# Kernel optimization log

Hardware: AMD Instinct MI355X
Metric: run time of the kernel (lower is better)

## Reference

```python
import jax, jax.numpy as jnp
import numpy as np

N = 50000
NEG_SLOPE = 0.2

def _gat_layer(x, src, dst, W, a_src, a_dst, b):
    # x: [N, Fin], W: [Fin, Fout], a_src/a_dst: [Fout], b: [Fout]
    h = x @ W                                  # [N, Fout]
    alpha_src = h @ a_src                      # [N]
    alpha_dst = h @ a_dst                      # [N]
    e = alpha_src[src] + alpha_dst[dst]        # [E]
    e = jnp.where(e > 0, e, NEG_SLOPE * e)     # leaky_relu
    # segment softmax over incoming edges of each dst node
    m = jax.ops.segment_max(e, dst, num_segments=N)
    w = jnp.exp(e - m[dst])
    denom = jax.ops.segment_sum(w, dst, num_segments=N) + jnp.asarray(1e-16, e.dtype)
    alpha = w / denom[dst]                     # [E]
    out = jax.ops.segment_sum(alpha[:, None] * h[src], dst, num_segments=N)
    return out + b

def setup_inputs() -> dict:
    key = jax.random.key(0)
    ks = jax.random.split(key, 10)
    x = jax.random.normal(ks[0], (N, 128), dtype=jnp.float32)
    edge_index = jax.random.randint(ks[1], (2, 800000), 0, N, dtype=jnp.int64)
    def glorot(k, shape):
        fan = shape[0] + (shape[1] if len(shape) > 1 else 1)
        s = jnp.sqrt(6.0 / fan)
        return jax.random.uniform(k, shape, jnp.float32, -s, s)
    return {
        "x": x,
        "edge_index": edge_index,
        "W1": glorot(ks[2], (128, 64)),
        "a1_src": glorot(ks[3], (64,)),
        "a1_dst": glorot(ks[4], (64,)),
        "b1": jnp.zeros((64,), jnp.float32),
        "W2": glorot(ks[5], (64, 64)),
        "a2_src": glorot(ks[6], (64,)),
        "a2_dst": glorot(ks[7], (64,)),
        "b2": jnp.zeros((64,), jnp.float32),
    }

def reference(x, edge_index, W1, a1_src, a1_dst, b1, W2, a2_src, a2_dst, b2):
    loops = jnp.arange(N, dtype=edge_index.dtype)
    src = jnp.concatenate([edge_index[0], loops])  # add self-loops (PyG default)
    dst = jnp.concatenate([edge_index[1], loops])
    h = _gat_layer(x, src, dst, W1, a1_src, a1_dst, b1)
    h = jax.nn.relu(h)
    out = _gat_layer(h, src, dst, W2, a2_src, a2_dst, b2)
    return out
```

## Files before the change

kernel.cpp:

```cpp
#include <hip/hip_runtime.h>
#include <hip/hip_bf16.h>
#include <hip/hip_fp16.h>
#include <cstddef>


#define NNODES 50000
#define NEDGES 800000
#define FOUT   64
#define NBKT   512
#define BSPAN  98
#define CHUNK  4096
#define REGS   2560
#define NLBMAX 256

__device__ __forceinline__ float leaky(float t) { return t > 0.f ? t : 0.2f * t; }
#define RL(v, j) __builtin_amdgcn_readlane((v), (j))

using half8  = __attribute__((ext_vector_type(8))) _Float16;
using half4v = __attribute__((ext_vector_type(4))) _Float16;
using f32x4  = __attribute__((ext_vector_type(4))) float;


__global__ __launch_bounds__(256) void k_localsort(
    const int* __restrict__ ei, unsigned* __restrict__ gout,
    int* __restrict__ goff, int E)
{
    __shared__ unsigned lrec[CHUNK];
    __shared__ unsigned lsrt[CHUNK];
    __shared__ int cnt[NBKT];
    __shared__ int cur[NBKT];
    __shared__ int exc[NBKT + 1];

    const int t = threadIdx.x;
    const int blk = blockIdx.x;
    const int e0 = blk * CHUNK;
    const int e1 = min(e0 + CHUNK, E);
    const int ne = e1 - e0;

    for (int i = t; i < NBKT; i += 256) cnt[i] = 0;
    __syncthreads();

    for (int i = e0 + t; i < e1; i += 256) {
        unsigned s = (unsigned)ei[i];
        unsigned d = (unsigned)ei[E + i];
        lrec[i - e0] = s | (d << 16);
        atomicAdd(&cnt[d / BSPAN], 1);
    }
    __syncthreads();

    if (t < 64) {
        int c[8]; int s = 0;
        #pragma unroll
        for (int k = 0; k < 8; ++k) { c[k] = cnt[t * 8 + k]; s += c[k]; }
        int inc = s;
        #pragma unroll
        for (int d = 1; d < 64; d <<= 1) { int u = __shfl_up(inc, d); if (t >= d) inc += u; }
        int ex = inc - s;
        #pragma unroll
        for (int k = 0; k < 8; ++k) { exc[t * 8 + k] = ex; cur[t * 8 + k] = ex; ex += c[k]; }
        if (t == 63) exc[NBKT] = ex;
    }
    __syncthreads();

    for (int i = t; i < ne; i += 256) {
        unsigned r = lrec[i];
        unsigned d = r >> 16;
        unsigned b = d / BSPAN;
        int p = atomicAdd(&cur[b], 1);
        lsrt[p] = (r & 0xFFFFu) | ((d - b * BSPAN) << 16);
    }
    __syncthreads();

    for (int i = t; i < ne; i += 256) gout[e0 + i] = lsrt[i];
    for (int i = t; i < NBKT + 1; i += 256)
        goff[blk * (NBKT + 1) + i] = e0 + exc[i];
}


__device__ __forceinline__ void csr_body(
    char* smem, int bkt,
    const unsigned* __restrict__ gout, const int* __restrict__ goff,
    int* __restrict__ csrc, int2* __restrict__ rowse,
    int n, int nlb)
{
    unsigned* ltmp  = (unsigned*)smem;
    int* lout  = (int*)(smem + REGS * 4);
    int* lcnt  = (int*)(smem + 2 * REGS * 4);
    int* lbase = lcnt + BSPAN;
    int* lcur  = lbase + BSPAN + 1;
    int* rg0   = lcur + BSPAN;
    int* rlen  = rg0 + NLBMAX;
    int* rbase = rlen + NLBMAX;

    const int t = threadIdx.x;
    const int node0 = bkt * BSPAN;
    if (node0 >= n) return;
    const int nn = min(BSPAN, n - node0);

    for (int i = t; i < BSPAN; i += 256) lcnt[i] = (i < nn) ? 1 : 0;
    if (t < nlb) {
        int g0 = goff[t * (NBKT + 1) + bkt];
        int g1 = goff[t * (NBKT + 1) + bkt + 1];
        rg0[t] = g0;
        rlen[t] = g1 - g0;
    }
    __syncthreads();

    if (t < 64) {
        int c[4]; int s = 0;
        #pragma unroll
        for (int k = 0; k < 4; ++k) {
            int idx = t * 4 + k;
            c[k] = (idx < nlb) ? rlen[idx] : 0;
            s += c[k];
        }
        int inc = s;
        #pragma unroll
        for (int d = 1; d < 64; d <<= 1) { int u = __shfl_up(inc, d); if (t >= d) inc += u; }
        int ex = inc - s;
        #pragma unroll
        for (int k = 0; k < 4; ++k) { rbase[t * 4 + k] = ex; ex += c[k]; }
        if (t == 63) rbase[NLBMAX] = ex;
    }
    __syncthreads();

    const int tot = min(rbase[nlb], REGS - BSPAN);

    for (int i = t; i < tot; i += 256) {
        int lo = 0, hi = nlb;
        while (hi - lo > 1) {
            int mid = (lo + hi) >> 1;
            if (rbase[mid] <= i) lo = mid; else hi = mid;
        }
        ltmp[i] = gout[rg0[lo] + (i - rbase[lo])];
    }
    __syncthreads();

    for (int i = t; i < tot; i += 256) atomicAdd(&lcnt[ltmp[i] >> 16], 1);
    __syncthreads();

    if (t < 64) {
        int b0 = t * 2, b1 = t * 2 + 1;
        int c0 = (b0 < BSPAN) ? lcnt[b0] : 0;
        int c1 = (b1 < BSPAN) ? lcnt[b1] : 0;
        int s = c0 + c1;
        int inc = s;
        #pragma unroll
        for (int d = 1; d < 64; d <<= 1) { int u = __shfl_up(inc, d); if (t >= d) inc += u; }
        int ex = inc - s;
        if (b0 < BSPAN) { lbase[b0] = ex;      lcur[b0] = ex + 1; }
        if (b1 < BSPAN) { lbase[b1] = ex + c0; lcur[b1] = ex + c0 + 1; }
        if (t == 63) lbase[BSPAN] = inc;
    }
    __syncthreads();

    for (int i = t; i < nn; i += 256) lout[lbase[i]] = node0 + i;
    for (int i = t; i < tot; i += 256) {
        unsigned r = ltmp[i];
        int p = atomicAdd(&lcur[r >> 16], 1);
        lout[p] = (int)(r & 0xFFFFu);
    }
    __syncthreads();

    const int gbase = bkt * REGS;
    const int total = tot + nn;
    for (int i = t; i < total; i += 256) csrc[gbase + i] = lout[i];
    for (int i = t; i < nn; i += 256)
        rowse[node0 + i] = make_int2(gbase + lbase[i], gbase + lbase[i + 1]);
}


template <int K, typename XT>
__device__ __forceinline__ void gemm_body(
    char* smem, int bx,
    const XT* __restrict__ x, const float* __restrict__ W,
    const float* __restrict__ a_src, const float* __restrict__ a_dst,
    __half* __restrict__ h16, float* __restrict__ as_, float* __restrict__ ad_, int n)
{
    constexpr int KP = K + 8;
    _Float16* Ah = (_Float16*)smem;
    _Float16* Wf = (_Float16*)(smem + 64 * KP * 2);

    const int t    = threadIdx.x;
    const int lane = t & 63;
    const int wv   = t >> 6;
    const int n16  = lane & 15;
    const int quad = lane >> 4;
    const int r0   = bx * 64;

    for (int i = t; i < K * 64; i += 256) {
        int k = i >> 6, c = i & 63;
        Wf[((k >> 3) * 64 + c) * 8 + (k & 7)] = (_Float16)W[i];
    }
    if constexpr (sizeof(XT) == 4) {
        constexpr int KQ = K / 4;
        for (int i = t; i < 64 * KQ; i += 256) {
            int r = i / KQ, kq = i % KQ;
            int row = r0 + r;
            float4 v = make_float4(0.f, 0.f, 0.f, 0.f);
            if (row < n) v = ((const float4*)(x + (size_t)row * K))[kq];
            half4v hv = { (_Float16)v.x, (_Float16)v.y, (_Float16)v.z, (_Float16)v.w };
            *(half4v*)&Ah[r * KP + kq * 4] = hv;
        }
    } else {
        constexpr int KO = K / 8;
        for (int i = t; i < 64 * KO; i += 256) {
            int r = i / KO, ko = i % KO;
            int row = r0 + r;
            half8 hv = {};
            if (row < n) hv = *(const half8*)((const _Float16*)x + (size_t)row * K + ko * 8);
            *(half8*)&Ah[r * KP + ko * 8] = hv;
        }
    }
    __syncthreads();

    half8 bfr[K / 32][4];
    #pragma unroll
    for (int kk = 0; kk < K / 32; ++kk)
        #pragma unroll
        for (int ct = 0; ct < 4; ++ct)
            bfr[kk][ct] = *(const half8*)&Wf[((kk * 4 + quad) * 64 + ct * 16 + n16) * 8];

    f32x4 acc[4];
    #pragma unroll
    for (int ct = 0; ct < 4; ++ct) acc[ct] = (f32x4){0.f, 0.f, 0.f, 0.f};

    #pragma unroll
    for (int kk = 0; kk < K / 32; ++kk) {
        half8 a = *(const half8*)&Ah[(wv * 16 + n16) * KP + kk * 32 + quad * 8];
        #pragma unroll
        for (int ct = 0; ct < 4; ++ct)
            acc[ct] = __builtin_amdgcn_mfma_f32_16x16x32_f16(a, bfr[kk][ct], acc[ct], 0, 0, 0);
    }

    const int rowb = r0 + wv * 16 + quad * 4;
    float asv[4], adv[4];
    #pragma unroll
    for (int ct = 0; ct < 4; ++ct) {
        asv[ct] = a_src[ct * 16 + n16];
        adv[ct] = a_dst[ct * 16 + n16];
    }
    float pa[4] = {0.f, 0.f, 0.f, 0.f}, pd[4] = {0.f, 0.f, 0.f, 0.f};
    #pragma unroll
    for (int ct = 0; ct < 4; ++ct)
        #pragma unroll
        for (int r = 0; r < 4; ++r) {
            pa[r] = fmaf(acc[ct][r], asv[ct], pa[r]);
            pd[r] = fmaf(acc[ct][r], adv[ct], pd[r]);
        }
    #pragma unroll
    for (int r = 0; r < 4; ++r) {
        #pragma unroll
        for (int d = 1; d <= 8; d <<= 1) {
            pa[r] += __shfl_xor(pa[r], d);
            pd[r] += __shfl_xor(pd[r], d);
        }
    }
    if (n16 == 0) {
        #pragma unroll
        for (int r = 0; r < 4; ++r) {
            if (rowb + r < n) { as_[rowb + r] = pa[r]; ad_[rowb + r] = pd[r]; }
        }
    }

    _Float16* hh = (_Float16*)h16;
    #pragma unroll
    for (int r = 0; r < 4; ++r) {
        if (rowb + r < n) {
            #pragma unroll
            for (int ct = 0; ct < 4; ++ct)
                hh[(size_t)(rowb + r) * 64 + ct * 16 + n16] = (_Float16)acc[ct][r];
        }
    }
}


__global__ __launch_bounds__(256) void k_csr_gemm1(
    const unsigned* __restrict__ gout, const int* __restrict__ goff,
    int* __restrict__ csrc, int2* __restrict__ rowse, int nlb,
    const float* __restrict__ x, const float* __restrict__ W1,
    const float* __restrict__ a1s, const float* __restrict__ a1d,
    __half* __restrict__ h16, float* __restrict__ as_, float* __restrict__ ad_, int n)
{
    extern __shared__ __align__(16) char smem[];
    if (blockIdx.x < NBKT)
        csr_body(smem, blockIdx.x, gout, goff, csrc, rowse, n, nlb);
    else
        gemm_body<128, float>(smem, blockIdx.x - NBKT, x, W1, a1s, a1d, h16, as_, ad_, n);
}

__global__ __launch_bounds__(256) void k_gemm2(
    const __half* __restrict__ xh, const float* __restrict__ W2,
    const float* __restrict__ a2s, const float* __restrict__ a2d,
    __half* __restrict__ h16, float* __restrict__ as_, float* __restrict__ ad_, int n)
{
    extern __shared__ __align__(16) char smem[];
    gemm_body<64, _Float16>(smem, blockIdx.x, (const _Float16*)xh, W2, a2s, a2d, h16, as_, ad_, n);
}


template <bool RELU, typename OT>
__device__ __forceinline__ void agg_one(
    int node, int lane, int2* __restrict__ swrow,
    const int2* __restrict__ rowse,
    const int* __restrict__ csrc, const __half* __restrict__ h16,
    const float* __restrict__ as_, const float* __restrict__ ad_,
    const float* __restrict__ bias, OT* __restrict__ out)
{
    const int2 se = rowse[node];
    const int start = se.x;
    const int end   = se.y;
    const int deg   = end - start;
    const float adn = ad_[node];

    if (deg <= 64) {
        int s = 0;
        if (lane < deg) s = csrc[start + lane];
        swrow[lane].x = s << 6;

        const int g  = lane >> 3;
        const int fl = (lane & 7) << 3;
        const __half* __restrict__ hf = h16 + fl;
        const int niter = (deg + 7) >> 3;

        int sofs[8];
        uint4 v[8];
        #pragma unroll
        for (int j = 0; j < 8; ++j) {
            if (j < niter) {
                sofs[j] = swrow[(j << 3) + g].x;
                v[j] = *(const uint4*)(hf + sofs[j]);
            }
        }

        float e = -1e30f;
        if (lane < deg) e = leaky(as_[s] + adn);
        float w = __expf(e);
        float dsum = w;
        #pragma unroll
        for (int d = 32; d >= 1; d >>= 1) dsum += __shfl_xor(dsum, d);
        swrow[lane].y = __float_as_int(w);

        float af[8] = {0.f, 0.f, 0.f, 0.f, 0.f, 0.f, 0.f, 0.f};
        #pragma unroll
        for (int j = 0; j < 8; ++j) {
            if (j < niter) {
                float wj = __int_as_float(swrow[(j << 3) + g].y);
                unsigned uu[4] = {v[j].x, v[j].y, v[j].z, v[j].w};
                #pragma unroll
                for (int q = 0; q < 4; ++q) {
                    __half2 h2 = *(__half2*)&uu[q];
                    float2 f2 = __half22float2(h2);
                    af[2 * q]     = fmaf(wj, f2.x, af[2 * q]);
                    af[2 * q + 1] = fmaf(wj, f2.y, af[2 * q + 1]);
                }
            }
        }
        #pragma unroll
        for (int q = 0; q < 8; ++q) {
            af[q] += __shfl_xor(af[q], 8);
            af[q] += __shfl_xor(af[q], 16);
            af[q] += __shfl_xor(af[q], 32);
        }
        if (g == 0) {
            float inv = 1.f / dsum;
            float4 b0 = *(const float4*)(bias + fl);
            float4 b1 = *(const float4*)(bias + fl + 4);
            float o[8] = { fmaf(af[0], inv, b0.x), fmaf(af[1], inv, b0.y),
                           fmaf(af[2], inv, b0.z), fmaf(af[3], inv, b0.w),
                           fmaf(af[4], inv, b1.x), fmaf(af[5], inv, b1.y),
                           fmaf(af[6], inv, b1.z), fmaf(af[7], inv, b1.w) };
            if (RELU) {
                #pragma unroll
                for (int q = 0; q < 8; ++q) o[q] = fmaxf(o[q], 0.f);
            }
            if constexpr (sizeof(OT) == 2) {
                __half* op = (__half*)out + (size_t)node * 64 + fl;
                __half2 p0 = __floats2half2_rn(o[0], o[1]);
                __half2 p1 = __floats2half2_rn(o[2], o[3]);
                __half2 p2 = __floats2half2_rn(o[4], o[5]);
                __half2 p3 = __floats2half2_rn(o[6], o[7]);
                uint4 pk = { *(unsigned*)&p0, *(unsigned*)&p1, *(unsigned*)&p2, *(unsigned*)&p3 };
                *(uint4*)op = pk;
            } else {
                float* op = (float*)out + (size_t)node * 64 + fl;
                *(float4*)op       = make_float4(o[0], o[1], o[2], o[3]);
                *(float4*)(op + 4) = make_float4(o[4], o[5], o[6], o[7]);
            }
        }
    } else {
        const __half* __restrict__ hp = h16 + lane;
        float m = -1e30f;
        for (int base = start; base < end; base += 64) {
            int idx = base + lane;
            if (idx < end) m = fmaxf(m, leaky(as_[csrc[idx]] + adn));
        }
        #pragma unroll
        for (int d = 32; d >= 1; d >>= 1) m = fmaxf(m, __shfl_xor(m, d));

        float acc0 = 0.f, acc1 = 0.f, acc2 = 0.f, acc3 = 0.f, dsum = 0.f;
        for (int base = start; base < end; base += 64) {
            int idx = base + lane;
            int s = 0; float w = 0.f;
            if (idx < end) {
                s = csrc[idx];
                w = __expf(leaky(as_[s] + adn) - m);
            }
            dsum += w;
            int off = s << 6;
            int wu = __float_as_uint(w);
            int cnt = min(64, end - base);
            int cr = (cnt + 3) & ~3;
            for (int j = 0; j < cr; j += 4) {
                int   o0 = RL(off, j + 0), o1 = RL(off, j + 1);
                int   o2 = RL(off, j + 2), o3 = RL(off, j + 3);
                float w0 = __uint_as_float(RL(wu, j + 0));
                float w1 = __uint_as_float(RL(wu, j + 1));
                float w2 = __uint_as_float(RL(wu, j + 2));
                float w3 = __uint_as_float(RL(wu, j + 3));
                float v0 = __half2float(hp[o0]), v1 = __half2float(hp[o1]);
                float v2 = __half2float(hp[o2]), v3 = __half2float(hp[o3]);
                acc0 = fmaf(w0, v0, acc0);
                acc1 = fmaf(w1, v1, acc1);
                acc2 = fmaf(w2, v2, acc2);
                acc3 = fmaf(w3, v3, acc3);
            }
        }
        #pragma unroll
        for (int d = 32; d >= 1; d >>= 1) dsum += __shfl_xor(dsum, d);
        float acc = (acc0 + acc1) + (acc2 + acc3);
        float o = acc / dsum + bias[lane];
        if (RELU) o = fmaxf(o, 0.f);
        if constexpr (sizeof(OT) == 2)
            ((__half*)out)[(size_t)node * 64 + lane] = __float2half(o);
        else
            ((float*)out)[(size_t)node * 64 + lane] = o;
    }
}

template <bool RELU, typename OT>
__global__ __launch_bounds__(256) void k_aggregate(
    const int2* __restrict__ rowse,
    const int* __restrict__ csrc,
    const __half* __restrict__ h16, const float* __restrict__ as_,
    const float* __restrict__ ad_, const float* __restrict__ bias,
    OT* __restrict__ out, int n)
{
    __shared__ int2 swL[4][64];

    const int lane = threadIdx.x & 63;
    const int wid  = threadIdx.x >> 6;
    const int nodeA = (blockIdx.x * 4 + wid) * 2;
    if (nodeA >= n) return;

    const int half = lane >> 5;
    const int hl   = lane & 31;
    const int node = nodeA + half;

    const int2 se = rowse[node];
    const float adn = ad_[node];
    const int start = se.x;
    const int deg   = se.y - se.x;
    const int mdeg  = max(deg, __shfl_xor(deg, 32));

    if (mdeg <= 32) {
        int s = 0;
        const bool act = hl < deg;
        if (act) s = csrc[start + hl];
        swL[wid][lane].x = s << 6;

        const int g  = (lane >> 3) & 3;
        const int fl = (lane & 7) << 3;
        const __half* __restrict__ hf = h16 + fl;
        int nit = (deg + 3) >> 2;
        nit = max(nit, __shfl_xor(nit, 32));

        const int sbase = (half << 5) + g;
        uint4 v[8];
        #pragma unroll
        for (int j = 0; j < 8; ++j) {
            if (j < nit)
                v[j] = *(const uint4*)(hf + swL[wid][sbase + (j << 2)].x);
        }

        float e = -1e30f;
        if (act) e = leaky(as_[s] + adn);
        float w = __expf(e);
        float dsum = w;
        #pragma unroll
        for (int d = 16; d >= 1; d >>= 1) dsum += __shfl_xor(dsum, d);
        swL[wid][lane].y = __float_as_int(w);

        float af[8] = {0.f, 0.f, 0.f, 0.f, 0.f, 0.f, 0.f, 0.f};
        #pragma unroll
        for (int j = 0; j < 8; ++j) {
            if (j < nit) {
                float wj = __int_as_float(swL[wid][sbase + (j << 2)].y);
                unsigned uu[4] = {v[j].x, v[j].y, v[j].z, v[j].w};
                #pragma unroll
                for (int q = 0; q < 4; ++q) {
                    __half2 h2 = *(__half2*)&uu[q];
                    float2 f2 = __half22float2(h2);
                    af[2 * q]     = fmaf(wj, f2.x, af[2 * q]);
                    af[2 * q + 1] = fmaf(wj, f2.y, af[2 * q + 1]);
                }
            }
        }
        #pragma unroll
        for (int q = 0; q < 8; ++q) {
            af[q] += __shfl_xor(af[q], 8);
            af[q] += __shfl_xor(af[q], 16);
        }
        if (g == 0) {
            float inv = 1.f / dsum;
            float4 b0 = *(const float4*)(bias + fl);
            float4 b1 = *(const float4*)(bias + fl + 4);
            float o[8] = { fmaf(af[0], inv, b0.x), fmaf(af[1], inv, b0.y),
                           fmaf(af[2], inv, b0.z), fmaf(af[3], inv, b0.w),
                           fmaf(af[4], inv, b1.x), fmaf(af[5], inv, b1.y),
                           fmaf(af[6], inv, b1.z), fmaf(af[7], inv, b1.w) };
            if (RELU) {
                #pragma unroll
                for (int q = 0; q < 8; ++q) o[q] = fmaxf(o[q], 0.f);
            }
            if constexpr (sizeof(OT) == 2) {
                __half* op = (__half*)out + (size_t)node * 64 + fl;
                __half2 p0 = __floats2half2_rn(o[0], o[1]);
                __half2 p1 = __floats2half2_rn(o[2], o[3]);
                __half2 p2 = __floats2half2_rn(o[4], o[5]);
                __half2 p3 = __floats2half2_rn(o[6], o[7]);
                uint4 pk = { *(unsigned*)&p0, *(unsigned*)&p1, *(unsigned*)&p2, *(unsigned*)&p3 };
                *(uint4*)op = pk;
            } else {
                float* op = (float*)out + (size_t)node * 64 + fl;
                *(float4*)op       = make_float4(o[0], o[1], o[2], o[3]);
                *(float4*)(op + 4) = make_float4(o[4], o[5], o[6], o[7]);
            }
        }
    } else {
        agg_one<RELU, OT>(nodeA,     lane, swL[wid], rowse, csrc, h16, as_, ad_, bias, out);
        agg_one<RELU, OT>(nodeA + 1, lane, swL[wid], rowse, csrc, h16, as_, ad_, bias, out);
    }
}


extern "C" void kernel_launch(void* const* d_in, const int* in_sizes, int n_in,
                              void* d_out, int out_size, void* d_ws, size_t ws_size,
                              hipStream_t stream) {
    const float* x   = (const float*)d_in[0];
    const int*   ei  = (const int*)  d_in[1];
    const float* W1  = (const float*)d_in[2];
    const float* a1s = (const float*)d_in[3];
    const float* a1d = (const float*)d_in[4];
    const float* b1  = (const float*)d_in[5];
    const float* W2  = (const float*)d_in[6];
    const float* a2s = (const float*)d_in[7];
    const float* a2d = (const float*)d_in[8];
    const float* b2  = (const float*)d_in[9];
    float* out = (float*)d_out;

    const int N_ = NNODES, E_ = NEDGES;
    const int NLB = (E_ + CHUNK - 1) / CHUNK;

    char* ws = (char*)d_ws;
    size_t off = 0;
    auto alloc = [&](size_t bytes) -> void* {
        void* p = ws + off;
        off += (bytes + 255) & ~(size_t)255;
        return p;
    };
    int*      csrc     = (int*)alloc((size_t)NBKT * REGS * 4);
    int2*     rowse    = (int2*)alloc((size_t)N_ * 8);
    float*    as_      = (float*)alloc((size_t)N_ * 4);
    float*    ad_      = (float*)alloc((size_t)N_ * 4);
    __half*   h16      = (__half*)alloc((size_t)N_ * FOUT * 2);
    __half*   xr2h     = (__half*)alloc((size_t)N_ * FOUT * 2);
    unsigned* gout     = (unsigned*)alloc((size_t)E_ * 4);
    int*      goff     = (int*)alloc((size_t)NLB * (NBKT + 1) * 4);

    constexpr unsigned SM_G1 = 64 * (128 + 8) * 2 + 128 * 64 * 2;
    constexpr unsigned SM_G2 = 64 * (64 + 8) * 2  + 64 * 64 * 2;

    const int GB = (N_ + 63) / 64;
    const int AB = (N_ / 2 + 3) / 4;

    k_localsort<<<NLB, 256, 0, stream>>>(ei, gout, goff, E_);
    k_csr_gemm1<<<NBKT + GB, 256, SM_G1, stream>>>(gout, goff, csrc, rowse, NLB,
                                                   x, W1, a1s, a1d, h16, as_, ad_, N_);
    k_aggregate<true,  __half><<<AB, 256, 0, stream>>>(rowse, csrc, h16, as_, ad_, b1, xr2h, N_);
    k_gemm2<<<GB, 256, SM_G2, stream>>>(xr2h, W2, a2s, a2d, h16, as_, ad_, N_);
    k_aggregate<false, float ><<<AB, 256, 0, stream>>>(rowse, csrc, h16, as_, ad_, b2, out, N_);
}
```

Before: 154.3 us.

## Fuse layer-1 aggregation with layer-2 GEMM via LDS tile and MFMA

Replaces the separate layer-1 aggregate and gemm2 kernels with one kernel. Each block aggregates 64 nodes into an fp16 LDS tile, then multiplies that tile by W2 with MFMA and computes the layer-2 attention scalars in the same pass. This removes the global round trip of the intermediate features and one launch. It also packs two low-degree nodes per wave, with half-wave processing when both have degree at most 32, to improve lane utilisation. In exchange, each block is fixed to 64 nodes, which may reduce occupancy or load balance compared with the previous aggregate grid.

```diff
diff --git a/kernel.cpp b/kernel.cpp
--- a/kernel.cpp
+++ b/kernel.cpp
@@ -289,29 +289,15 @@
         gemm_body<128, float>(smem, blockIdx.x - NBKT, x, W1, a1s, a1d, h16, as_, ad_, n);
 }
 
-__global__ __launch_bounds__(256) void k_gemm2(
-    const __half* __restrict__ xh, const float* __restrict__ W2,
-    const float* __restrict__ a2s, const float* __restrict__ a2d,
-    __half* __restrict__ h16, float* __restrict__ as_, float* __restrict__ ad_, int n)
+
+__device__ __forceinline__ void agg_one_lds(
+    int rloc, int start, int end, float adn, int lane, int2* __restrict__ swrow,
+    const int* __restrict__ csrc, const __half* __restrict__ h16,
+    const float* __restrict__ as_, const float* __restrict__ bias,
+    _Float16* __restrict__ Ah)
 {
-    extern __shared__ __align__(16) char smem[];
-    gemm_body<64, _Float16>(smem, blockIdx.x, (const _Float16*)xh, W2, a2s, a2d, h16, as_, ad_, n);
-}
-
-
-template <bool RELU, typename OT>
-__device__ __forceinline__ void agg_one(
-    int node, int lane, int2* __restrict__ swrow,
-    const int2* __restrict__ rowse,
-    const int* __restrict__ csrc, const __half* __restrict__ h16,
-    const float* __restrict__ as_, const float* __restrict__ ad_,
-    const float* __restrict__ bias, OT* __restrict__ out)
-{
-    const int2 se = rowse[node];
-    const int start = se.x;
-    const int end   = se.y;
-    const int deg   = end - start;
-    const float adn = ad_[node];
+    constexpr int KP = 72;
+    const int deg = end - start;
 
     if (deg <= 64) {
         int s = 0;
@@ -323,15 +309,10 @@
         const __half* __restrict__ hf = h16 + fl;
         const int niter = (deg + 7) >> 3;
 
-        int sofs[8];
         uint4 v[8];
         #pragma unroll
-        for (int j = 0; j < 8; ++j) {
-            if (j < niter) {
-                sofs[j] = swrow[(j << 3) + g].x;
-                v[j] = *(const uint4*)(hf + sofs[j]);
-            }
-        }
+        for (int j = 0; j < 8; ++j)
+            if (j < niter) v[j] = *(const uint4*)(hf + swrow[(j << 3) + g].x);
 
         float e = -1e30f;
         if (lane < deg) e = leaky(as_[s] + adn);
@@ -370,23 +351,11 @@
                            fmaf(af[2], inv, b0.z), fmaf(af[3], inv, b0.w),
                            fmaf(af[4], inv, b1.x), fmaf(af[5], inv, b1.y),
                            fmaf(af[6], inv, b1.z), fmaf(af[7], inv, b1.w) };
-            if (RELU) {
-                #pragma unroll
-                for (int q = 0; q < 8; ++q) o[q] = fmaxf(o[q], 0.f);
-            }
-            if constexpr (sizeof(OT) == 2) {
-                __half* op = (__half*)out + (size_t)node * 64 + fl;
-                __half2 p0 = __floats2half2_rn(o[0], o[1]);
-                __half2 p1 = __floats2half2_rn(o[2], o[3]);
-                __half2 p2 = __floats2half2_rn(o[4], o[5]);
-                __half2 p3 = __floats2half2_rn(o[6], o[7]);
-                uint4 pk = { *(unsigned*)&p0, *(unsigned*)&p1, *(unsigned*)&p2, *(unsigned*)&p3 };
-                *(uint4*)op = pk;
-            } else {
-                float* op = (float*)out + (size_t)node * 64 + fl;
-                *(float4*)op       = make_float4(o[0], o[1], o[2], o[3]);
-                *(float4*)(op + 4) = make_float4(o[4], o[5], o[6], o[7]);
-            }
+            half8 st = { (_Float16)fmaxf(o[0], 0.f), (_Float16)fmaxf(o[1], 0.f),
+                         (_Float16)fmaxf(o[2], 0.f), (_Float16)fmaxf(o[3], 0.f),
+                         (_Float16)fmaxf(o[4], 0.f), (_Float16)fmaxf(o[5], 0.f),
+                         (_Float16)fmaxf(o[6], 0.f), (_Float16)fmaxf(o[7], 0.f) };
+            *(half8*)&Ah[rloc * KP + fl] = st;
         }
     } else {
         const __half* __restrict__ hp = h16 + lane;
@@ -430,6 +399,324 @@
         for (int d = 32; d >= 1; d >>= 1) dsum += __shfl_xor(dsum, d);
         float acc = (acc0 + acc1) + (acc2 + acc3);
         float o = acc / dsum + bias[lane];
+        Ah[rloc * KP + lane] = (_Float16)fmaxf(o, 0.f);
+    }
+}
+
+
+__global__ __launch_bounds__(256) void k_agg1_gemm2(
+    const int2* __restrict__ rowse, const int* __restrict__ csrc,
+    const __half* __restrict__ h1, const float* __restrict__ as1,
+    const float* __restrict__ ad1, const float* __restrict__ bias1,
+    const float* __restrict__ W2, const float* __restrict__ a2s,
+    const float* __restrict__ a2d, __half* __restrict__ h2,
+    float* __restrict__ as2, float* __restrict__ ad2, int n)
+{
+    constexpr int KP = 72;
+    __shared__ _Float16 Ah[64 * KP];
+    __shared__ _Float16 Wf[64 * 64];
+    __shared__ int2 swL[4][64];
+
+    const int t    = threadIdx.x;
+    const int lane = t & 63;
+    const int wv   = t >> 6;
+    const int r0   = blockIdx.x * 64;
+
+    for (int i = t; i < 64 * 64; i += 256) {
+        int k = i >> 6, c = i & 63;
+        Wf[((k >> 3) * 64 + c) * 8 + (k & 7)] = (_Float16)W2[i];
+    }
+    if (r0 + 64 > n) {
+        for (int i = t; i < 64 * KP; i += 256) Ah[i] = (_Float16)0.f;
+    }
+    __syncthreads();
+
+    const int half = lane >> 5;
+    const int hl   = lane & 31;
+
+    int2  myse = make_int2(0, 0);
+    float myad = 0.f;
+    {
+        int nd = r0 + wv * 16 + lane;
+        if (lane < 16 && nd < n) { myse = rowse[nd]; myad = ad1[nd]; }
+    }
+
+    for (int it = 0; it < 8; ++it) {
+        const int pbase = r0 + wv * 16 + it * 2;
+        if (pbase >= n) break;
+        const int idx   = it * 2 + half;
+        const int start = __shfl(myse.x, idx);
+        const int end   = __shfl(myse.y, idx);
+        const float adn = __shfl(myad, idx);
+        const int deg   = end - start;
+        const int rloc  = wv * 16 + it * 2 + half;
+        const int mdeg  = max(deg, __shfl_xor(deg, 32));
+
+        if (mdeg <= 32) {
+            int s = 0;
+            const bool act = hl < deg;
+            if (act) s = csrc[start + hl];
+            swL[wv][lane].x = s << 6;
+
+            const int g  = (lane >> 3) & 3;
+            const int fl = (lane & 7) << 3;
+            const __half* __restrict__ hf = h1 + fl;
+            int nit = (deg + 3) >> 2;
+            nit = max(nit, __shfl_xor(nit, 32));
+
+            const int sbase = (half << 5) + g;
+            uint4 v[8];
+            #pragma unroll
+            for (int j = 0; j < 8; ++j)
+                if (j < nit) v[j] = *(const uint4*)(hf + swL[wv][sbase + (j << 2)].x);
+
+            float e = -1e30f;
+            if (act) e = leaky(as1[s] + adn);
+            float w = __expf(e);
+            float dsum = w;
+            #pragma unroll
+            for (int d = 16; d >= 1; d >>= 1) dsum += __shfl_xor(dsum, d);
+            swL[wv][lane].y = __float_as_int(w);
+
+            float af[8] = {0.f, 0.f, 0.f, 0.f, 0.f, 0.f, 0.f, 0.f};
+            #pragma unroll
+            for (int j = 0; j < 8; ++j) {
+                if (j < nit) {
+                    float wj = __int_as_float(swL[wv][sbase + (j << 2)].y);
+                    unsigned uu[4] = {v[j].x, v[j].y, v[j].z, v[j].w};
+                    #pragma unroll
+                    for (int q = 0; q < 4; ++q) {
+                        __half2 hh2 = *(__half2*)&uu[q];
+                        float2 f2 = __half22float2(hh2);
+                        af[2 * q]     = fmaf(wj, f2.x, af[2 * q]);
+                        af[2 * q + 1] = fmaf(wj, f2.y, af[2 * q + 1]);
+                    }
+                }
+            }
+            #pragma unroll
+            for (int q = 0; q < 8; ++q) {
+                af[q] += __shfl_xor(af[q], 8);
+                af[q] += __shfl_xor(af[q], 16);
+            }
+            if (g == 0) {
+                float inv = 1.f / dsum;
+                float4 b0 = *(const float4*)(bias1 + fl);
+                float4 b1 = *(const float4*)(bias1 + fl + 4);
+                float o[8] = { fmaf(af[0], inv, b0.x), fmaf(af[1], inv, b0.y),
+                               fmaf(af[2], inv, b0.z), fmaf(af[3], inv, b0.w),
+                               fmaf(af[4], inv, b1.x), fmaf(af[5], inv, b1.y),
+                               fmaf(af[6], inv, b1.z), fmaf(af[7], inv, b1.w) };
+                half8 st = { (_Float16)fmaxf(o[0], 0.f), (_Float16)fmaxf(o[1], 0.f),
+                             (_Float16)fmaxf(o[2], 0.f), (_Float16)fmaxf(o[3], 0.f),
+                             (_Float16)fmaxf(o[4], 0.f), (_Float16)fmaxf(o[5], 0.f),
+                             (_Float16)fmaxf(o[6], 0.f), (_Float16)fmaxf(o[7], 0.f) };
+                *(half8*)&Ah[rloc * KP + fl] = st;
+            }
+        } else {
+            int   sA = __shfl(myse.x, it * 2),     eA = __shfl(myse.y, it * 2);
+            int   sB = __shfl(myse.x, it * 2 + 1), eB = __shfl(myse.y, it * 2 + 1);
+            float aA = __shfl(myad, it * 2),       aB = __shfl(myad, it * 2 + 1);
+            agg_one_lds(wv * 16 + it * 2,     sA, eA, aA, lane, swL[wv], csrc, h1, as1, bias1, Ah);
+            agg_one_lds(wv * 16 + it * 2 + 1, sB, eB, aB, lane, swL[wv], csrc, h1, as1, bias1, Ah);
+        }
+    }
+    __syncthreads();
+
+    const int n16  = lane & 15;
+    const int quad = lane >> 4;
+
+    half8 bfr[2][4];
+    #pragma unroll
+    for (int kk = 0; kk < 2; ++kk)
+        #pragma unroll
+        for (int ct = 0; ct < 4; ++ct)
+            bfr[kk][ct] = *(const half8*)&Wf[((kk * 4 + quad) * 64 + ct * 16 + n16) * 8];
+
+    f32x4 acc[4];
+    #pragma unroll
+    for (int ct = 0; ct < 4; ++ct) acc[ct] = (f32x4){0.f, 0.f, 0.f, 0.f};
+
+    #pragma unroll
+    for (int kk = 0; kk < 2; ++kk) {
+        half8 a = *(const half8*)&Ah[(wv * 16 + n16) * KP + kk * 32 + quad * 8];
+        #pragma unroll
+        for (int ct = 0; ct < 4; ++ct)
+            acc[ct] = __builtin_amdgcn_mfma_f32_16x16x32_f16(a, bfr[kk][ct], acc[ct], 0, 0, 0);
+    }
+
+    const int rowb = r0 + wv * 16 + quad * 4;
+    float asv[4], adv[4];
+    #pragma unroll
+    for (int ct = 0; ct < 4; ++ct) {
+        asv[ct] = a2s[ct * 16 + n16];
+        adv[ct] = a2d[ct * 16 + n16];
+    }
+    float pa[4] = {0.f, 0.f, 0.f, 0.f}, pd[4] = {0.f, 0.f, 0.f, 0.f};
+    #pragma unroll
+    for (int ct = 0; ct < 4; ++ct)
+        #pragma unroll
+        for (int r = 0; r < 4; ++r) {
+            pa[r] = fmaf(acc[ct][r], asv[ct], pa[r]);
+            pd[r] = fmaf(acc[ct][r], adv[ct], pd[r]);
+        }
+    #pragma unroll
+    for (int r = 0; r < 4; ++r) {
+        #pragma unroll
+        for (int d = 1; d <= 8; d <<= 1) {
+            pa[r] += __shfl_xor(pa[r], d);
+            pd[r] += __shfl_xor(pd[r], d);
+        }
+    }
+    if (n16 == 0) {
+        #pragma unroll
+        for (int r = 0; r < 4; ++r) {
+            if (rowb + r < n) { as2[rowb + r] = pa[r]; ad2[rowb + r] = pd[r]; }
+        }
+    }
+
+    _Float16* hh = (_Float16*)h2;
+    #pragma unroll
+    for (int r = 0; r < 4; ++r) {
+        if (rowb + r < n) {
+            #pragma unroll
+            for (int ct = 0; ct < 4; ++ct)
+                hh[(size_t)(rowb + r) * 64 + ct * 16 + n16] = (_Float16)acc[ct][r];
+        }
+    }
+}
+
+
+template <bool RELU, typename OT>
+__device__ __forceinline__ void agg_one(
+    int node, int lane, int2* __restrict__ swrow,
+    const int2* __restrict__ rowse,
+    const int* __restrict__ csrc, const __half* __restrict__ h16,
+    const float* __restrict__ as_, const float* __restrict__ ad_,
+    const float* __restrict__ bias, OT* __restrict__ out)
+{
+    const int2 se = rowse[node];
+    const int start = se.x;
+    const int end   = se.y;
+    const int deg   = end - start;
+    const float adn = ad_[node];
+
+    if (deg <= 64) {
+        int s = 0;
+        if (lane < deg) s = csrc[start + lane];
+        swrow[lane].x = s << 6;
+
+        const int g  = lane >> 3;
+        const int fl = (lane & 7) << 3;
+        const __half* __restrict__ hf = h16 + fl;
+        const int niter = (deg + 7) >> 3;
+
+        int sofs[8];
+        uint4 v[8];
+        #pragma unroll
+        for (int j = 0; j < 8; ++j) {
+            if (j < niter) {
+                sofs[j] = swrow[(j << 3) + g].x;
+                v[j] = *(const uint4*)(hf + sofs[j]);
+            }
+        }
+
+        float e = -1e30f;
+        if (lane < deg) e = leaky(as_[s] + adn);
+        float w = __expf(e);
+        float dsum = w;
+        #pragma unroll
+        for (int d = 32; d >= 1; d >>= 1) dsum += __shfl_xor(dsum, d);
+        swrow[lane].y = __float_as_int(w);
+
+        float af[8] = {0.f, 0.f, 0.f, 0.f, 0.f, 0.f, 0.f, 0.f};
+        #pragma unroll
+        for (int j = 0; j < 8; ++j) {
+            if (j < niter) {
+                float wj = __int_as_float(swrow[(j << 3) + g].y);
+                unsigned uu[4] = {v[j].x, v[j].y, v[j].z, v[j].w};
+                #pragma unroll
+                for (int q = 0; q < 4; ++q) {
+                    __half2 h2 = *(__half2*)&uu[q];
+                    float2 f2 = __half22float2(h2);
+                    af[2 * q]     = fmaf(wj, f2.x, af[2 * q]);
+                    af[2 * q + 1] = fmaf(wj, f2.y, af[2 * q + 1]);
+                }
+            }
+        }
+        #pragma unroll
+        for (int q = 0; q < 8; ++q) {
+            af[q] += __shfl_xor(af[q], 8);
+            af[q] += __shfl_xor(af[q], 16);
+            af[q] += __shfl_xor(af[q], 32);
+        }
+        if (g == 0) {
+            float inv = 1.f / dsum;
+            float4 b0 = *(const float4*)(bias + fl);
+            float4 b1 = *(const float4*)(bias + fl + 4);
+            float o[8] = { fmaf(af[0], inv, b0.x), fmaf(af[1], inv, b0.y),
+                           fmaf(af[2], inv, b0.z), fmaf(af[3], inv, b0.w),
+                           fmaf(af[4], inv, b1.x), fmaf(af[5], inv, b1.y),
+                           fmaf(af[6], inv, b1.z), fmaf(af[7], inv, b1.w) };
+            if (RELU) {
+                #pragma unroll
+                for (int q = 0; q < 8; ++q) o[q] = fmaxf(o[q], 0.f);
+            }
+            if constexpr (sizeof(OT) == 2) {
+                __half* op = (__half*)out + (size_t)node * 64 + fl;
+                __half2 p0 = __floats2half2_rn(o[0], o[1]);
+                __half2 p1 = __floats2half2_rn(o[2], o[3]);
+                __half2 p2 = __floats2half2_rn(o[4], o[5]);
+                __half2 p3 = __floats2half2_rn(o[6], o[7]);
+                uint4 pk = { *(unsigned*)&p0, *(unsigned*)&p1, *(unsigned*)&p2, *(unsigned*)&p3 };
+                *(uint4*)op = pk;
+            } else {
+                float* op = (float*)out + (size_t)node * 64 + fl;
+                *(float4*)op       = make_float4(o[0], o[1], o[2], o[3]);
+                *(float4*)(op + 4) = make_float4(o[4], o[5], o[6], o[7]);
+            }
+        }
+    } else {
+        const __half* __restrict__ hp = h16 + lane;
+        float m = -1e30f;
+        for (int base = start; base < end; base += 64) {
+            int idx = base + lane;
+            if (idx < end) m = fmaxf(m, leaky(as_[csrc[idx]] + adn));
+        }
+        #pragma unroll
+        for (int d = 32; d >= 1; d >>= 1) m = fmaxf(m, __shfl_xor(m, d));
+
+        float acc0 = 0.f, acc1 = 0.f, acc2 = 0.f, acc3 = 0.f, dsum = 0.f;
+        for (int base = start; base < end; base += 64) {
+            int idx = base + lane;
+            int s = 0; float w = 0.f;
+            if (idx < end) {
+                s = csrc[idx];
+                w = __expf(leaky(as_[s] + adn) - m);
+            }
+            dsum += w;
+            int off = s << 6;
+            int wu = __float_as_uint(w);
+            int cnt = min(64, end - base);
+            int cr = (cnt + 3) & ~3;
+            for (int j = 0; j < cr; j += 4) {
+                int   o0 = RL(off, j + 0), o1 = RL(off, j + 1);
+                int   o2 = RL(off, j + 2), o3 = RL(off, j + 3);
+                float w0 = __uint_as_float(RL(wu, j + 0));
+                float w1 = __uint_as_float(RL(wu, j + 1));
+                float w2 = __uint_as_float(RL(wu, j + 2));
+                float w3 = __uint_as_float(RL(wu, j + 3));
+                float v0 = __half2float(hp[o0]), v1 = __half2float(hp[o1]);
+                float v2 = __half2float(hp[o2]), v3 = __half2float(hp[o3]);
+                acc0 = fmaf(w0, v0, acc0);
+                acc1 = fmaf(w1, v1, acc1);
+                acc2 = fmaf(w2, v2, acc2);
+                acc3 = fmaf(w3, v3, acc3);
+            }
+        }
+        #pragma unroll
+        for (int d = 32; d >= 1; d >>= 1) dsum += __shfl_xor(dsum, d);
+        float acc = (acc0 + acc1) + (acc2 + acc3);
+        float o = acc / dsum + bias[lane];
         if (RELU) o = fmaxf(o, 0.f);
         if constexpr (sizeof(OT) == 2)
             ((__half*)out)[(size_t)node * 64 + lane] = __float2half(o);
@@ -573,13 +860,14 @@
     int2*     rowse    = (int2*)alloc((size_t)N_ * 8);
     float*    as_      = (float*)alloc((size_t)N_ * 4);
     float*    ad_      = (float*)alloc((size_t)N_ * 4);
+    float*    as2      = (float*)alloc((size_t)N_ * 4);
+    float*    ad2      = (float*)alloc((size_t)N_ * 4);
     __half*   h16      = (__half*)alloc((size_t)N_ * FOUT * 2);
-    __half*   xr2h     = (__half*)alloc((size_t)N_ * FOUT * 2);
+    __half*   h2       = (__half*)alloc((size_t)N_ * FOUT * 2);
     unsigned* gout     = (unsigned*)alloc((size_t)E_ * 4);
     int*      goff     = (int*)alloc((size_t)NLB * (NBKT + 1) * 4);
 
     constexpr unsigned SM_G1 = 64 * (128 + 8) * 2 + 128 * 64 * 2;
-    constexpr unsigned SM_G2 = 64 * (64 + 8) * 2  + 64 * 64 * 2;
 
     const int GB = (N_ + 63) / 64;
     const int AB = (N_ / 2 + 3) / 4;
@@ -587,7 +875,7 @@
     k_localsort<<<NLB, 256, 0, stream>>>(ei, gout, goff, E_);
     k_csr_gemm1<<<NBKT + GB, 256, SM_G1, stream>>>(gout, goff, csrc, rowse, NLB,
                                                    x, W1, a1s, a1d, h16, as_, ad_, N_);
-    k_aggregate<true,  __half><<<AB, 256, 0, stream>>>(rowse, csrc, h16, as_, ad_, b1, xr2h, N_);
-    k_gemm2<<<GB, 256, SM_G2, stream>>>(xr2h, W2, a2s, a2d, h16, as_, ad_, N_);
-    k_aggregate<false, float ><<<AB, 256, 0, stream>>>(rowse, csrc, h16, as_, ad_, b2, out, N_);
+    k_agg1_gemm2<<<GB, 256, 0, stream>>>(rowse, csrc, h16, as_, ad_, b1,
+                                         W2, a2s, a2d, h2, as2, ad2, N_);
+    k_aggregate<false, float><<<AB, 256, 0, stream>>>(rowse, csrc, h2, as2, ad2, b2, out, N_);
 }
```

Result: slower. 167.9 us (+8.8%).
